# Kernel optimization log

Measured on AMD Instinct MI355X. Metric: run time of the kernel, lower is better.

The kernel has to match this reference:

```python
import jax, jax.numpy as jnp
import numpy as np

HADAMARD_DIM = 4096  # power of 2 -> had_rem_dim is None, rem_dim = 1


def _fwht(x):
    """Fast Walsh-Hadamard transform along last dim (natural/Sylvester order).

    x: [B, n] with n a power of 2. Returns x @ H_n (unnormalized).
    Mirrors QuaRot's recursive butterfly: at each stage, pairs are split into
    (a+b) and (a-b) halves. log2(n) stages, each O(n) work per row.
    """
    bsz, n = x.shape
    steps = int(np.log2(n))
    u = x[:, :, None]  # [B, n, 1]
    m = n
    for _ in range(steps):  # fixed-trip loop over log2(n) stages, jit-friendly
        u = u.reshape(bsz, m // 2, 2, -1)
        a = u[:, :, 0, :]
        b = u[:, :, 1, :]
        u = jnp.concatenate([a + b, a - b], axis=-1)  # [B, m//2, 2k]
        m //= 2
    return u.reshape(bsz, n)


def matmul_hadU(x):
    """QuaRot matmul_hadU for power-of-2 dim: normalized FWHT, 1/sqrt(n)."""
    n = x.shape[-1]
    flat = x.reshape(-1, n)
    out = _fwht(flat) * (1.0 / np.sqrt(n))
    return out.reshape(x.shape).astype(x.dtype)


def setup_inputs() -> dict:
    key = jax.random.key(0)
    x = jax.random.normal(key, (8192, HADAMARD_DIM), dtype=jnp.float32)
    return {"x": x}


def reference(x):
    # FWHT.forward: x -> matmul_hadU_cuda(x, None, 1) -> cast back to x.dtype
    return matmul_hadU(x)
```

## Files before the change

### kernel.cpp

```cpp
#include <hip/hip_runtime.h>


#define N        4096
#define THREADS  64
#define LDS_FLOATS 4096

__device__ __forceinline__ void fwht64(float v[64]) {
#pragma unroll
    for (int s = 1; s < 64; s <<= 1) {
#pragma unroll
        for (int k = 0; k < 64; k++) {
            if ((k & s) == 0) {
                float a = v[k];
                float b = v[k + s];
                v[k]     = a + b;
                v[k + s] = a - b;
            }
        }
    }
}

__global__ __launch_bounds__(THREADS)
void FWHT_83476984365427_kernel(const float* __restrict__ x,
                                float* __restrict__ out,
                                int nrows) {
    __shared__ float lds[LDS_FLOATS];

    const int row = blockIdx.x;
    if (row >= nrows) return;

    const float* __restrict__ xr  = x   + (size_t)row * N;
    float* __restrict__       otr = out + (size_t)row * N;
    const int l  = threadIdx.x;
    const int lh = l >> 4;
    const int ls = l & 15;

#pragma unroll
    for (int i = 0; i < 16; i++) {
        const int hi = 4 * i + lh;
        const int hm = 4 * (i & 3) + lh;
        const int c  = ls ^ hm;
        const float* src = xr + hi * 64 + c * 4;
        __builtin_amdgcn_global_load_lds(
            (const __attribute__((address_space(1))) void*)src,
            (__attribute__((address_space(3))) void*)(&lds[i * 256]),
            16, 0, 0);
    }
    asm volatile("s_waitcnt vmcnt(0)" ::: "memory");
    __syncthreads();

    float v[64];

    {
        const float* rowp = &lds[l * 64];
#pragma unroll
        for (int c = 0; c < 16; c++) {
            float4 f = *(const float4*)(rowp + ((c ^ ls) << 2));
            v[4 * c + 0] = f.x;
            v[4 * c + 1] = f.y;
            v[4 * c + 2] = f.z;
            v[4 * c + 3] = f.w;
        }
    }

    fwht64(v);

    {
        float* rowp = &lds[l * 64];
#pragma unroll
        for (int c = 0; c < 16; c++) {
            float4 f;
            f.x = v[4 * c + 0];
            f.y = v[4 * c + 1];
            f.z = v[4 * c + 2];
            f.w = v[4 * c + 3];
            *(float4*)(rowp + ((c ^ ls) << 2)) = f;
        }
    }
    __syncthreads();

    {
        const int l2 = l >> 2;
        const int j  = l & 3;
#pragma unroll
        for (int ml = 0; ml < 16; ml++) {
            const int off = ((l2 ^ ml) << 2) + j;
#pragma unroll
            for (int mh = 0; mh < 4; mh++) {
                v[mh * 16 + ml] = lds[(mh * 16 + ml) * 64 + off];
            }
        }
    }

    fwht64(v);

    const float scale = 1.0f / 64.0f;
#pragma unroll
    for (int m = 0; m < 64; m++) otr[m * 64 + l] = v[m] * scale;
}

extern "C" void kernel_launch(void* const* d_in, const int* in_sizes, int n_in,
                              void* d_out, int out_size, void* d_ws, size_t ws_size,
                              hipStream_t stream) {
    (void)n_in; (void)d_ws; (void)ws_size; (void)out_size;
    const float* x = (const float*)d_in[0];
    float* out = (float*)d_out;
    const int nrows = in_sizes[0] / N;
    dim3 grid(nrows);
    dim3 block(THREADS);
    FWHT_83476984365427_kernel<<<grid, block, 0, stream>>>(x, out, nrows);
}
```

Before: 229.3 us.

## Process four rows per block with double-buffered LDS prefetch of next row

Each workgroup now handles four rows and prefetches the next row into a second LDS buffer via global_load_lds while transforming the current row. Barriers are replaced with waitcnt instructions since the block is a single wave. This aims to hide global load latency behind compute, but doubles LDS per block, which lowers the number of resident waves per CU and reduces the number of blocks.

```diff
diff --git a/kernel.cpp b/kernel.cpp
--- a/kernel.cpp
+++ b/kernel.cpp
@@ -3,7 +3,8 @@
 
 #define N        4096
 #define THREADS  64
-#define LDS_FLOATS 4096
+#define RPB      4
+#define BUF_FLOATS 4096
 
 __device__ __forceinline__ void fwht64(float v[64]) {
 #pragma unroll
@@ -24,79 +25,95 @@
 void FWHT_83476984365427_kernel(const float* __restrict__ x,
                                 float* __restrict__ out,
                                 int nrows) {
-    __shared__ float lds[LDS_FLOATS];
+    __shared__ float lds[2][BUF_FLOATS];
 
-    const int row = blockIdx.x;
-    if (row >= nrows) return;
+    const int r0 = blockIdx.x * RPB;
+    if (r0 >= nrows) return;
 
-    const float* __restrict__ xr  = x   + (size_t)row * N;
-    float* __restrict__       otr = out + (size_t)row * N;
     const int l  = threadIdx.x;
     const int lh = l >> 4;
     const int ls = l & 15;
 
+    auto STAGE = [&](int row, int buf) {
+        const float* __restrict__ xr = x + (size_t)row * N;
 #pragma unroll
-    for (int i = 0; i < 16; i++) {
-        const int hi = 4 * i + lh;
-        const int hm = 4 * (i & 3) + lh;
-        const int c  = ls ^ hm;
-        const float* src = xr + hi * 64 + c * 4;
-        __builtin_amdgcn_global_load_lds(
-            (const __attribute__((address_space(1))) void*)src,
-            (__attribute__((address_space(3))) void*)(&lds[i * 256]),
-            16, 0, 0);
-    }
-    asm volatile("s_waitcnt vmcnt(0)" ::: "memory");
-    __syncthreads();
+        for (int i = 0; i < 16; i++) {
+            const int hi = 4 * i + lh;
+            const int hm = 4 * (i & 3) + lh;
+            const int c  = ls ^ hm;
+            const float* src = xr + hi * 64 + c * 4;
+            __builtin_amdgcn_global_load_lds(
+                (const __attribute__((address_space(1))) void*)src,
+                (__attribute__((address_space(3))) void*)(&lds[buf][i * 256]),
+                16, 0, 0);
+        }
+    };
 
-    float v[64];
+    STAGE(r0, 0);
 
-    {
-        const float* rowp = &lds[l * 64];
+    for (int j = 0; j < RPB; j++) {
+        const int row = r0 + j;
+        if (row >= nrows) break;
+        const int cur = j & 1;
+
+        if (j == 0) asm volatile("s_waitcnt vmcnt(0)" ::: "memory");
+        else        asm volatile("s_waitcnt vmcnt(63)" ::: "memory");
+
+        if (j + 1 < RPB && row + 1 < nrows) STAGE(row + 1, cur ^ 1);
+
+        float v[64];
+        const float* __restrict__ bp = &lds[cur][0];
+
+        {
+            const float* rowp = bp + l * 64;
 #pragma unroll
-        for (int c = 0; c < 16; c++) {
-            float4 f = *(const float4*)(rowp + ((c ^ ls) << 2));
-            v[4 * c + 0] = f.x;
-            v[4 * c + 1] = f.y;
-            v[4 * c + 2] = f.z;
-            v[4 * c + 3] = f.w;
+            for (int c = 0; c < 16; c++) {
+                float4 f = *(const float4*)(rowp + ((c ^ ls) << 2));
+                v[4 * c + 0] = f.x;
+                v[4 * c + 1] = f.y;
+                v[4 * c + 2] = f.z;
+                v[4 * c + 3] = f.w;
+            }
+        }
+
+        fwht64(v);
+
+        {
+            float* rowp = (float*)bp + l * 64;
+#pragma unroll
+            for (int c = 0; c < 16; c++) {
+                float4 f;
+                f.x = v[4 * c + 0];
+                f.y = v[4 * c + 1];
+                f.z = v[4 * c + 2];
+                f.w = v[4 * c + 3];
+                *(float4*)(rowp + ((c ^ ls) << 2)) = f;
+            }
+        }
+        asm volatile("s_waitcnt lgkmcnt(0)" ::: "memory");
+
+        {
+            const int l2 = l >> 2;
+            const int jj = l & 3;
+#pragma unroll
+            for (int ml = 0; ml < 16; ml++) {
+                const int off = ((l2 ^ ml) << 2) + jj;
+#pragma unroll
+                for (int mh = 0; mh < 4; mh++) {
+                    v[mh * 16 + ml] = bp[(mh * 16 + ml) * 64 + off];
+                }
+            }
+        }
+
+        fwht64(v);
+
+        {
+            float* __restrict__ otr = out + (size_t)row * N;
+            const float scale = 1.0f / 64.0f;
+#pragma unroll
+            for (int m = 0; m < 64; m++) otr[m * 64 + l] = v[m] * scale;
         }
     }
-
-    fwht64(v);
-
-    {
-        float* rowp = &lds[l * 64];
-#pragma unroll
-        for (int c = 0; c < 16; c++) {
-            float4 f;
-            f.x = v[4 * c + 0];
-            f.y = v[4 * c + 1];
-            f.z = v[4 * c + 2];
-            f.w = v[4 * c + 3];
-            *(float4*)(rowp + ((c ^ ls) << 2)) = f;
-        }
-    }
-    __syncthreads();
-
-    {
-        const int l2 = l >> 2;
-        const int j  = l & 3;
-#pragma unroll
-        for (int ml = 0; ml < 16; ml++) {
-            const int off = ((l2 ^ ml) << 2) + j;
-#pragma unroll
-            for (int mh = 0; mh < 4; mh++) {
-                v[mh * 16 + ml] = lds[(mh * 16 + ml) * 64 + off];
-            }
-        }
-    }
-
-    fwht64(v);
-
-    const float scale = 1.0f / 64.0f;
-#pragma unroll
-    for (int m = 0; m < 64; m++) otr[m * 64 + l] = v[m] * scale;
 }
 
 extern "C" void kernel_launch(void* const* d_in, const int* in_sizes, int n_in,
@@ -106,7 +123,7 @@
     const float* x = (const float*)d_in[0];
     float* out = (float*)d_out;
     const int nrows = in_sizes[0] / N;
-    dim3 grid(nrows);
+    dim3 grid((nrows + RPB - 1) / RPB);
     dim3 block(THREADS);
     FWHT_83476984365427_kernel<<<grid, block, 0, stream>>>(x, out, nrows);
 }
```

New measurement: 239.9 us. +4.6%, slower.
